# Kernel optimization log

Measured on AMD Instinct MI355X. Metric: run time of the kernel, lower is better.

## Reference

```python
import jax, jax.numpy as jnp
import numpy as np

N = 100000   # nodes
E = 1600000  # edges
G = 512      # graphs in batch
F_IN = 30
H = 128
EPS = 1e-5   # BatchNorm1d default eps


def setup_inputs() -> dict:
    key = jax.random.key(0)
    ks = jax.random.split(key, 16)
    x = jax.random.normal(ks[0], (N, F_IN), dtype=jnp.float32)
    edge_index = jax.random.randint(ks[1], (2, E), 0, N, dtype=jnp.int64)
    batch = jnp.sort(jax.random.randint(ks[2], (N,), 0, G, dtype=jnp.int64))
    d = {"x": x, "edge_index": edge_index, "batch": batch}
    dims = [(F_IN, H), (H, H), (H, H)]
    for i, (din, dout) in enumerate(dims):
        d[f"W{i}"] = jax.random.normal(ks[3 + i], (din, dout), dtype=jnp.float32) * (1.0 / np.sqrt(din))
        d[f"b{i}"] = jnp.zeros((dout,), dtype=jnp.float32)
        d[f"g{i}"] = jnp.ones((dout,), dtype=jnp.float32)   # BN gamma
        d[f"bt{i}"] = jnp.zeros((dout,), dtype=jnp.float32)  # BN beta
    d["HW1"] = jax.random.normal(ks[9], (H, 64), dtype=jnp.float32) * (1.0 / np.sqrt(H))
    d["Hb1"] = jnp.zeros((64,), dtype=jnp.float32)
    d["HW2"] = jax.random.normal(ks[10], (64, 1), dtype=jnp.float32) * 0.125
    d["Hb2"] = jnp.zeros((1,), dtype=jnp.float32)
    return d


def _bn(x, gamma, beta):
    # training-mode BatchNorm1d over node dim, biased variance (as torch uses for normalization)
    mu = jnp.mean(x, axis=0)
    var = jnp.mean(jnp.square(x - mu), axis=0)
    return (x - mu) * jax.lax.rsqrt(var + EPS) * gamma + beta


def reference(x, edge_index, batch, W0, b0, g0, bt0, W1, b1, g1, bt1, W2, b2, g2, bt2, HW1, Hb1, HW2, Hb2):
    # GCNConv: add self-loops, symmetric D^{-1/2}(A+I)D^{-1/2} normalization
    loop = jnp.arange(N, dtype=edge_index.dtype)
    src = jnp.concatenate([edge_index[0], loop])  # [E+N]
    dst = jnp.concatenate([edge_index[1], loop])
    deg = jax.ops.segment_sum(jnp.ones(src.shape, jnp.float32), dst, num_segments=N)
    dinv = jax.lax.rsqrt(jnp.maximum(deg, 1.0))  # deg >= 1 due to self-loops
    norm = (dinv[src] * dinv[dst])[:, None]      # [E+N, 1]

    for W, b, g, bt in ((W0, b0, g0, bt0), (W1, b1, g1, bt1), (W2, b2, g2, bt2)):
        h = x @ W                                           # [N, H]
        agg = jax.ops.segment_sum(h[src] * norm, dst, num_segments=N) + b
        x = jnp.maximum(_bn(agg, g, bt), 0.0)               # BN + ReLU (dropout = identity here)

    # global_mean_pool over graph ids
    counts = jax.ops.segment_sum(jnp.ones((N,), jnp.float32), batch, num_segments=G)
    pooled = jax.ops.segment_sum(x, batch, num_segments=G) / jnp.maximum(counts, 1.0)[:, None]

    h = jnp.maximum(pooled @ HW1 + Hb1, 0.0)
    return (h @ HW2 + Hb2).squeeze(-1)  # [G]
```

## Files before the change

### kernel.cpp

```cpp
#include <hip/hip_runtime.h>

#define BN_EPS 1e-5f
#define BSH 8

typedef __attribute__((ext_vector_type(8))) short bf16x8;
typedef __attribute__((ext_vector_type(4))) float f32x4;

__device__ inline float bfhi(unsigned int v) { return __uint_as_float(v & 0xFFFF0000u); }
__device__ inline float bflo(unsigned int v) { return __uint_as_float(v << 16); }
__device__ inline unsigned short f2bf(float f) {
  unsigned int u = __float_as_uint(f);
  u += 0x7FFFu + ((u >> 16) & 1u);
  return (unsigned short)(u >> 16);
}
__device__ inline unsigned int pack2bf(float lo, float hi) {
  return (unsigned int)f2bf(lo) | ((unsigned int)f2bf(hi) << 16);
}

__global__ void k_prep(const int* __restrict__ src, const int* __restrict__ dst,
                       int* __restrict__ gcur, uint2* __restrict__ sedge,
                       int NB, int CAP, int E, int BB,
                       const float* __restrict__ x, const float* __restrict__ W0,
                       const float* __restrict__ W1, const float* __restrict__ W2,
                       unsigned short* __restrict__ xb, unsigned short* __restrict__ Wt0,
                       unsigned short* __restrict__ Wt1, unsigned short* __restrict__ Wt2,
                       int n) {
  if ((int)blockIdx.x < BB) {
    __shared__ int lh[512], rb[512];
    int tid = threadIdx.x;
    for (int i = tid; i < NB; i += 256) lh[i] = 0;
    __syncthreads();
    int base = blockIdx.x * 8192;
    int lim = min(8192, E - base);
    for (int i = tid; i < lim; i += 256)
      atomicAdd(&lh[dst[base + i] >> BSH], 1);
    __syncthreads();
    for (int i = tid; i < NB; i += 256) {
      int c = lh[i];
      rb[i] = c ? atomicAdd(&gcur[i], c) : 0;
      lh[i] = 0;
    }
    __syncthreads();
    for (int i = tid; i < lim; i += 256) {
      int d = dst[base + i];
      int s = src[base + i];
      int b = d >> BSH;
      int pos = rb[b] + atomicAdd(&lh[b], 1);
      if (pos < CAP) {
        uint2 v; v.x = (unsigned int)s; v.y = (unsigned int)d;
        sedge[(size_t)b * CAP + pos] = v;
      }
    }
  } else {
    int t0 = (((int)blockIdx.x - BB) * 256 + (int)threadIdx.x) * 4;
#pragma unroll
    for (int u = 0; u < 4; ++u) {
      int t = t0 + u;
      if (t < 4096) {
        int nn = t >> 5, k = t & 31;
        Wt0[t] = f2bf(k < 30 ? W0[k * 128 + nn] : 0.f);
      } else if (t < 20480) {
        int i = t - 4096; int nn = i >> 7, k = i & 127;
        Wt1[i] = f2bf(W1[k * 128 + nn]);
      } else if (t < 36864) {
        int i = t - 20480; int nn = i >> 7, k = i & 127;
        Wt2[i] = f2bf(W2[k * 128 + nn]);
      } else {
        int i = t - 36864;
        if (i < n * 32) {
          int row = i >> 5, c = i & 31;
          xb[i] = f2bf(c < 30 ? x[row * 30 + c] : 0.f);
        }
      }
    }
  }
}

__global__ void k_csr1(const uint2* __restrict__ sedge, const int* __restrict__ gcur,
                       int* __restrict__ startv, int* __restrict__ cnt,
                       float* __restrict__ dinv, int CAP, int n) {
  int b = blockIdx.x, tid = threadIdx.x;
  __shared__ int h[256], sc[256];
  if (tid < 256) h[tid] = 0;
  __syncthreads();
  int cb = gcur[b]; if (cb > CAP) cb = CAP;
  const uint2* sd = sedge + (size_t)b * CAP;
  for (int i = tid; i < cb; i += 1024) atomicAdd(&h[sd[i].y & 255], 1);
  __syncthreads();
  if (tid < 256) sc[tid] = h[tid];
  __syncthreads();
  for (int o = 1; o < 256; o <<= 1) {
    int t = (tid < 256 && tid >= o) ? sc[tid - o] : 0;
    __syncthreads();
    if (tid < 256) sc[tid] += t;
    __syncthreads();
  }
  if (tid < 256) {
    int gd = (b << BSH) + tid;
    if (gd < n) {
      int v = h[tid];
      startv[gd] = b * CAP + (sc[tid] - v);
      cnt[gd] = v;
      dinv[gd] = rsqrtf((float)v + 1.0f);
    }
  }
}

__global__ void k_csr2(const uint2* __restrict__ sedge, const int* __restrict__ gcur,
                       const int* __restrict__ startv, const float* __restrict__ dinv,
                       unsigned int* __restrict__ elist, int CAP, int n) {
  int b = blockIdx.x, tid = threadIdx.x;
  __shared__ int cur[256];
  if (tid < 256) {
    int gd = (b << BSH) + tid;
    cur[tid] = (gd < n) ? startv[gd] : 0;
  }
  __syncthreads();
  int cb = gcur[b]; if (cb > CAP) cb = CAP;
  const uint2* sd = sedge + (size_t)b * CAP;
  for (int i = tid; i < cb; i += 1024) {
    uint2 e = sd[i];
    int pos = atomicAdd(&cur[e.y & 255], 1);
    unsigned int u = (unsigned int)(dinv[e.x] * 32767.0f + 0.5f);
    elist[pos] = e.x | (u << 17);
  }
}

__global__ void k_gather0(const unsigned int* __restrict__ elist, const int* __restrict__ start,
                          const int* __restrict__ cnt, const float* __restrict__ dinv,
                          const uint4* __restrict__ x4,
                          unsigned int* __restrict__ G0, int n) {
  int lane = threadIdx.x & 63;
  int wv   = threadIdx.x >> 6;
  int grp  = lane >> 2;
  int q4   = lane & 3;
  int row  = blockIdx.x * 4 + wv;
  bool active = row < n;

  float acc[8];
  float di = 0.f, dq = 0.f;
  int len = 0;
  const unsigned int* ep = elist;
  if (active) {
    di = dinv[row];
    dq = di * (1.0f / 32767.0f);
    len = cnt[row];
    ep = elist + start[row];
  }
  {
    float selfw = (grp == 0 && active) ? di * di : 0.f;
    uint4 hv = (grp == 0 && active) ? x4[(size_t)row * 4 + q4] : make_uint4(0, 0, 0, 0);
    acc[0] = bflo(hv.x) * selfw; acc[1] = bfhi(hv.x) * selfw;
    acc[2] = bflo(hv.y) * selfw; acc[3] = bfhi(hv.y) * selfw;
    acc[4] = bflo(hv.z) * selfw; acc[5] = bfhi(hv.z) * selfw;
    acc[6] = bflo(hv.w) * selfw; acc[7] = bfhi(hv.w) * selfw;
  }
  int j = 0;
  for (; j + 32 <= len; j += 32) {
    unsigned int e0 = ep[j + grp];
    unsigned int e1 = ep[j + 16 + grp];
    uint4 v0 = x4[(size_t)(e0 & 0x1FFFFu) * 4 + q4];
    uint4 v1 = x4[(size_t)(e1 & 0x1FFFFu) * 4 + q4];
    float w0 = (float)(e0 >> 17) * dq;
    float w1 = (float)(e1 >> 17) * dq;
    acc[0] = fmaf(bflo(v0.x), w0, acc[0]); acc[1] = fmaf(bfhi(v0.x), w0, acc[1]);
    acc[2] = fmaf(bflo(v0.y), w0, acc[2]); acc[3] = fmaf(bfhi(v0.y), w0, acc[3]);
    acc[4] = fmaf(bflo(v0.z), w0, acc[4]); acc[5] = fmaf(bfhi(v0.z), w0, acc[5]);
    acc[6] = fmaf(bflo(v0.w), w0, acc[6]); acc[7] = fmaf(bfhi(v0.w), w0, acc[7]);
    acc[0] = fmaf(bflo(v1.x), w1, acc[0]); acc[1] = fmaf(bfhi(v1.x), w1, acc[1]);
    acc[2] = fmaf(bflo(v1.y), w1, acc[2]); acc[3] = fmaf(bfhi(v1.y), w1, acc[3]);
    acc[4] = fmaf(bflo(v1.z), w1, acc[4]); acc[5] = fmaf(bfhi(v1.z), w1, acc[5]);
    acc[6] = fmaf(bflo(v1.w), w1, acc[6]); acc[7] = fmaf(bfhi(v1.w), w1, acc[7]);
  }
  for (; j < len; j += 16) {
    int jj = j + grp;
    unsigned int e = (jj < len) ? ep[jj] : 0u;
    uint4 v = x4[(size_t)(e & 0x1FFFFu) * 4 + q4];
    float w = (float)(e >> 17) * dq;
    acc[0] = fmaf(bflo(v.x), w, acc[0]); acc[1] = fmaf(bfhi(v.x), w, acc[1]);
    acc[2] = fmaf(bflo(v.y), w, acc[2]); acc[3] = fmaf(bfhi(v.y), w, acc[3]);
    acc[4] = fmaf(bflo(v.z), w, acc[4]); acc[5] = fmaf(bfhi(v.z), w, acc[5]);
    acc[6] = fmaf(bflo(v.w), w, acc[6]); acc[7] = fmaf(bfhi(v.w), w, acc[7]);
  }
#pragma unroll
  for (int k = 0; k < 8; ++k) {
    acc[k] += __shfl_xor(acc[k], 4);
    acc[k] += __shfl_xor(acc[k], 8);
    acc[k] += __shfl_xor(acc[k], 16);
    acc[k] += __shfl_xor(acc[k], 32);
  }
  if (grp == 0 && active) {
    uint4 o;
    o.x = pack2bf(acc[0], acc[1]);
    o.y = pack2bf(acc[2], acc[3]);
    o.z = pack2bf(acc[4], acc[5]);
    o.w = pack2bf(acc[6], acc[7]);
    ((uint4*)G0)[(size_t)row * 4 + q4] = o;
  }
}

template <int KP, bool DOBN, bool DOSTATS>
__global__ void k_gemm_mfma(const unsigned short* __restrict__ A,
                            const unsigned short* __restrict__ Wt,
                            const float* __restrict__ bnIn, const float* __restrict__ gamma,
                            const float* __restrict__ beta,
                            const float* __restrict__ bias, float* __restrict__ bnslab,
                            unsigned short* __restrict__ C, int n) {
  __shared__ float ssc[128], ssh[128];
  if constexpr (DOBN) {
    __shared__ float red[256];
    int tid = threadIdx.x;
    int which = tid >> 7, c = tid & 127;
    float s = 0.f;
    for (int k = 0; k < 64; ++k) s += bnIn[k * 256 + which * 128 + c];
    red[tid] = s;
    __syncthreads();
    if (tid < 128) {
      float invn = 1.0f / (float)n;
      float mu  = red[tid] * invn;
      float var = fmaxf(red[128 + tid] * invn - mu * mu, 0.f);
      float sc  = gamma[tid] * rsqrtf(var + BN_EPS);
      ssc[tid] = sc;
      ssh[tid] = fmaf(-mu, sc, beta[tid]);
    }
    __syncthreads();
  }
  int wave = threadIdx.x >> 6;
  int lane = threadIdx.x & 63;
  int m0 = blockIdx.x * 128 + wave * 32;
  int lm = lane & 15;
  int lq = lane >> 4;

  f32x4 acc[2][8] = {};
  const unsigned short* Arow0 = A + (size_t)(m0 + lm) * KP + lq * 8;
  const unsigned short* Arow1 = Arow0 + (size_t)16 * KP;
  const unsigned short* Bbase = Wt + (size_t)lm * KP + lq * 8;

#pragma unroll
  for (int k0 = 0; k0 < KP; k0 += 32) {
    uint4 ra0 = *(const uint4*)(Arow0 + k0);
    uint4 ra1 = *(const uint4*)(Arow1 + k0);
    bf16x8 a0, a1;
    if constexpr (DOBN) {
      int cb = k0 + lq * 8;
      unsigned int w0 = pack2bf(fmaxf(fmaf(bflo(ra0.x), ssc[cb+0], ssh[cb+0]), 0.f),
                                fmaxf(fmaf(bfhi(ra0.x), ssc[cb+1], ssh[cb+1]), 0.f));
      unsigned int w1 = pack2bf(fmaxf(fmaf(bflo(ra0.y), ssc[cb+2], ssh[cb+2]), 0.f),
                                fmaxf(fmaf(bfhi(ra0.y), ssc[cb+3], ssh[cb+3]), 0.f));
      unsigned int w2 = pack2bf(fmaxf(fmaf(bflo(ra0.z), ssc[cb+4], ssh[cb+4]), 0.f),
                                fmaxf(fmaf(bfhi(ra0.z), ssc[cb+5], ssh[cb+5]), 0.f));
      unsigned int w3 = pack2bf(fmaxf(fmaf(bflo(ra0.w), ssc[cb+6], ssh[cb+6]), 0.f),
                                fmaxf(fmaf(bfhi(ra0.w), ssc[cb+7], ssh[cb+7]), 0.f));
      uint4 pa0 = make_uint4(w0, w1, w2, w3);
      a0 = *(bf16x8*)&pa0;
      unsigned int y0 = pack2bf(fmaxf(fmaf(bflo(ra1.x), ssc[cb+0], ssh[cb+0]), 0.f),
                                fmaxf(fmaf(bfhi(ra1.x), ssc[cb+1], ssh[cb+1]), 0.f));
      unsigned int y1 = pack2bf(fmaxf(fmaf(bflo(ra1.y), ssc[cb+2], ssh[cb+2]), 0.f),
                                fmaxf(fmaf(bfhi(ra1.y), ssc[cb+3], ssh[cb+3]), 0.f));
      unsigned int y2 = pack2bf(fmaxf(fmaf(bflo(ra1.z), ssc[cb+4], ssh[cb+4]), 0.f),
                                fmaxf(fmaf(bfhi(ra1.z), ssc[cb+5], ssh[cb+5]), 0.f));
      unsigned int y3 = pack2bf(fmaxf(fmaf(bflo(ra1.w), ssc[cb+6], ssh[cb+6]), 0.f),
                                fmaxf(fmaf(bfhi(ra1.w), ssc[cb+7], ssh[cb+7]), 0.f));
      uint4 pa1 = make_uint4(y0, y1, y2, y3);
      a1 = *(bf16x8*)&pa1;
    } else {
      a0 = *(bf16x8*)&ra0;
      a1 = *(bf16x8*)&ra1;
    }
#pragma unroll
    for (int t = 0; t < 8; ++t) {
      bf16x8 b = *(const bf16x8*)(Bbase + (size_t)t * 16 * KP + k0);
      acc[0][t] = __builtin_amdgcn_mfma_f32_16x16x32_bf16(a0, b, acc[0][t], 0, 0, 0);
      acc[1][t] = __builtin_amdgcn_mfma_f32_16x16x32_bf16(a1, b, acc[1][t], 0, 0, 0);
    }
  }

#pragma unroll
  for (int h = 0; h < 2; ++h) {
    int rbase = m0 + h * 16 + lq * 4;
#pragma unroll
    for (int t = 0; t < 8; ++t) {
      int col = t * 16 + lm;
      float bv = DOSTATS ? bias[col] : 0.f;
#pragma unroll
      for (int r = 0; r < 4; ++r) {
        int row = rbase + r;
        if (row < n) C[(size_t)row * 128 + col] = f2bf(acc[h][t][r] + bv);
      }
    }
  }

  if constexpr (DOSTATS) {
    __shared__ float sms[4][256];
#pragma unroll
    for (int t = 0; t < 8; ++t) {
      int col = t * 16 + lm;
      float bv = bias[col];
      float s = 0.f, s2 = 0.f;
#pragma unroll
      for (int h = 0; h < 2; ++h) {
        int rbase = m0 + h * 16 + lq * 4;
#pragma unroll
        for (int r = 0; r < 4; ++r) {
          if (rbase + r < n) {
            float v = acc[h][t][r] + bv;
            s += v; s2 = fmaf(v, v, s2);
          }
        }
      }
      s  += __shfl_xor(s, 16);  s  += __shfl_xor(s, 32);
      s2 += __shfl_xor(s2, 16); s2 += __shfl_xor(s2, 32);
      if (lq == 0) { sms[wave][col] = s; sms[wave][128 + col] = s2; }
    }
    __syncthreads();
    int tid = threadIdx.x;
    int slab = (blockIdx.x & 63) * 256;
    float tot = sms[0][tid] + sms[1][tid] + sms[2][tid] + sms[3][tid];
    atomicAdd(&bnslab[slab + tid], tot);
  }
}

__global__ void k_gather(const unsigned int* __restrict__ elist, const int* __restrict__ start,
                         const int* __restrict__ cnt, const float* __restrict__ dinv,
                         const uint4* __restrict__ h4,
                         const float* __restrict__ bias, unsigned int* __restrict__ agg,
                         float* __restrict__ bnsumP, int n) {
  int lane = threadIdx.x & 63;
  int wv   = threadIdx.x >> 6;
  int grp  = lane >> 4;
  int c8   = lane & 15;
  int row  = blockIdx.x * 4 + wv;
  bool active = row < n;

  float acc[8];
  float di = 0.f, dq = 0.f;
  int len = 0;
  const unsigned int* ep = elist;

  if (active) {
    di = dinv[row];
    dq = di * (1.0f / 32767.0f);
    len = cnt[row];
    ep = elist + start[row];
  }

  {
    float selfw = (grp == 0 && active) ? di * di : 0.f;
    float4 b0 = make_float4(0.f, 0.f, 0.f, 0.f), b1 = b0;
    if (grp == 0 && active) {
      b0 = ((const float4*)bias)[c8 * 2];
      b1 = ((const float4*)bias)[c8 * 2 + 1];
    }
    uint4 hv = active ? h4[(size_t)row * 16 + c8] : make_uint4(0, 0, 0, 0);
    acc[0] = fmaf(bflo(hv.x), selfw, b0.x);
    acc[1] = fmaf(bfhi(hv.x), selfw, b0.y);
    acc[2] = fmaf(bflo(hv.y), selfw, b0.z);
    acc[3] = fmaf(bfhi(hv.y), selfw, b0.w);
    acc[4] = fmaf(bflo(hv.z), selfw, b1.x);
    acc[5] = fmaf(bfhi(hv.z), selfw, b1.y);
    acc[6] = fmaf(bflo(hv.w), selfw, b1.z);
    acc[7] = fmaf(bfhi(hv.w), selfw, b1.w);
  }

  int j = 0;
  for (; j + 16 <= len; j += 16) {
    unsigned int e0 = ep[j + grp];
    unsigned int e1 = ep[j + 4 + grp];
    unsigned int e2 = ep[j + 8 + grp];
    unsigned int e3 = ep[j + 12 + grp];
    uint4 v0 = h4[(size_t)(e0 & 0x1FFFFu) * 16 + c8];
    uint4 v1 = h4[(size_t)(e1 & 0x1FFFFu) * 16 + c8];
    uint4 v2 = h4[(size_t)(e2 & 0x1FFFFu) * 16 + c8];
    uint4 v3 = h4[(size_t)(e3 & 0x1FFFFu) * 16 + c8];
    float w0 = (float)(e0 >> 17) * dq;
    float w1 = (float)(e1 >> 17) * dq;
    float w2 = (float)(e2 >> 17) * dq;
    float w3 = (float)(e3 >> 17) * dq;
    acc[0] = fmaf(bflo(v0.x), w0, acc[0]); acc[1] = fmaf(bfhi(v0.x), w0, acc[1]);
    acc[2] = fmaf(bflo(v0.y), w0, acc[2]); acc[3] = fmaf(bfhi(v0.y), w0, acc[3]);
    acc[4] = fmaf(bflo(v0.z), w0, acc[4]); acc[5] = fmaf(bfhi(v0.z), w0, acc[5]);
    acc[6] = fmaf(bflo(v0.w), w0, acc[6]); acc[7] = fmaf(bfhi(v0.w), w0, acc[7]);
    acc[0] = fmaf(bflo(v1.x), w1, acc[0]); acc[1] = fmaf(bfhi(v1.x), w1, acc[1]);
    acc[2] = fmaf(bflo(v1.y), w1, acc[2]); acc[3] = fmaf(bfhi(v1.y), w1, acc[3]);
    acc[4] = fmaf(bflo(v1.z), w1, acc[4]); acc[5] = fmaf(bfhi(v1.z), w1, acc[5]);
    acc[6] = fmaf(bflo(v1.w), w1, acc[6]); acc[7] = fmaf(bfhi(v1.w), w1, acc[7]);
    acc[0] = fmaf(bflo(v2.x), w2, acc[0]); acc[1] = fmaf(bfhi(v2.x), w2, acc[1]);
    acc[2] = fmaf(bflo(v2.y), w2, acc[2]); acc[3] = fmaf(bfhi(v2.y), w2, acc[3]);
    acc[4] = fmaf(bflo(v2.z), w2, acc[4]); acc[5] = fmaf(bfhi(v2.z), w2, acc[5]);
    acc[6] = fmaf(bflo(v2.w), w2, acc[6]); acc[7] = fmaf(bfhi(v2.w), w2, acc[7]);
    acc[0] = fmaf(bflo(v3.x), w3, acc[0]); acc[1] = fmaf(bfhi(v3.x), w3, acc[1]);
    acc[2] = fmaf(bflo(v3.y), w3, acc[2]); acc[3] = fmaf(bfhi(v3.y), w3, acc[3]);
    acc[4] = fmaf(bflo(v3.z), w3, acc[4]); acc[5] = fmaf(bfhi(v3.z), w3, acc[5]);
    acc[6] = fmaf(bflo(v3.w), w3, acc[6]); acc[7] = fmaf(bfhi(v3.w), w3, acc[7]);
  }
  for (; j + 8 <= len; j += 8) {
    unsigned int e0 = ep[j + grp];
    unsigned int e1 = ep[j + 4 + grp];
    uint4 v0 = h4[(size_t)(e0 & 0x1FFFFu) * 16 + c8];
    uint4 v1 = h4[(size_t)(e1 & 0x1FFFFu) * 16 + c8];
    float w0 = (float)(e0 >> 17) * dq;
    float w1 = (float)(e1 >> 17) * dq;
    acc[0] = fmaf(bflo(v0.x), w0, acc[0]); acc[1] = fmaf(bfhi(v0.x), w0, acc[1]);
    acc[2] = fmaf(bflo(v0.y), w0, acc[2]); acc[3] = fmaf(bfhi(v0.y), w0, acc[3]);
    acc[4] = fmaf(bflo(v0.z), w0, acc[4]); acc[5] = fmaf(bfhi(v0.z), w0, acc[5]);
    acc[6] = fmaf(bflo(v0.w), w0, acc[6]); acc[7] = fmaf(bfhi(v0.w), w0, acc[7]);
    acc[0] = fmaf(bflo(v1.x), w1, acc[0]); acc[1] = fmaf(bfhi(v1.x), w1, acc[1]);
    acc[2] = fmaf(bflo(v1.y), w1, acc[2]); acc[3] = fmaf(bfhi(v1.y), w1, acc[3]);
    acc[4] = fmaf(bflo(v1.z), w1, acc[4]); acc[5] = fmaf(bfhi(v1.z), w1, acc[5]);
    acc[6] = fmaf(bflo(v1.w), w1, acc[6]); acc[7] = fmaf(bfhi(v1.w), w1, acc[7]);
  }
  for (; j < len; j += 4) {
    int jj = j + grp;
    unsigned int e = (jj < len) ? ep[jj] : 0u;
    uint4 v = h4[(size_t)(e & 0x1FFFFu) * 16 + c8];
    float w = (float)(e >> 17) * dq;
    acc[0] = fmaf(bflo(v.x), w, acc[0]); acc[1] = fmaf(bfhi(v.x), w, acc[1]);
    acc[2] = fmaf(bflo(v.y), w, acc[2]); acc[3] = fmaf(bfhi(v.y), w, acc[3]);
    acc[4] = fmaf(bflo(v.z), w, acc[4]); acc[5] = fmaf(bfhi(v.z), w, acc[5]);
    acc[6] = fmaf(bflo(v.w), w, acc[6]); acc[7] = fmaf(bfhi(v.w), w, acc[7]);
  }

#pragma unroll
  for (int k = 0; k < 8; ++k) {
    acc[k] += __shfl_xor(acc[k], 16);
    acc[k] += __shfl_xor(acc[k], 32);
  }

  __shared__ float sm[2][4][128];
  if (lane < 16) {
    if (active) {
      uint4 o;
      o.x = pack2bf(acc[0], acc[1]);
      o.y = pack2bf(acc[2], acc[3]);
      o.z = pack2bf(acc[4], acc[5]);
      o.w = pack2bf(acc[6], acc[7]);
      ((uint4*)agg)[(size_t)row * 16 + c8] = o;
    }
#pragma unroll
    for (int k = 0; k < 8; ++k) {
      float a = acc[k];
      sm[0][wv][c8 * 8 + k] = a;
      sm[1][wv][c8 * 8 + k] = a * a;
    }
  }
  __syncthreads();
  int tid = threadIdx.x;
  int slab = (blockIdx.x & 63) * 256;
  if (tid < 128) {
    float s = sm[0][0][tid] + sm[0][1][tid] + sm[0][2][tid] + sm[0][3][tid];
    atomicAdd(&bnsumP[slab + tid], s);
  } else {
    int c = tid - 128;
    float s = sm[1][0][c] + sm[1][1][c] + sm[1][2][c] + sm[1][3][c];
    atomicAdd(&bnsumP[slab + 128 + c], s);
  }
}

__global__ void k_poolhead(const unsigned int* __restrict__ aggd, const float* __restrict__ bnIn,
                           const float* __restrict__ gamma, const float* __restrict__ beta,
                           const int* __restrict__ batch, const float* __restrict__ HW1,
                           const float* __restrict__ Hb1, const float* __restrict__ HW2,
                           const float* __restrict__ Hb2, float* __restrict__ out, int n) {
  __shared__ float bsc[128], bsh[128];
  {
    __shared__ float red[256];
    int tid = threadIdx.x;
    int which = tid >> 7, c = tid & 127;
    float s = 0.f;
    for (int k = 0; k < 64; ++k) s += bnIn[k * 256 + which * 128 + c];
    red[tid] = s;
    __syncthreads();
    if (tid < 128) {
      float invn = 1.0f / (float)n;
      float mu  = red[tid] * invn;
      float var = fmaxf(red[128 + tid] * invn - mu * mu, 0.f);
      float sc  = gamma[tid] * rsqrtf(var + BN_EPS);
      bsc[tid] = sc;
      bsh[tid] = fmaf(-mu, sc, beta[tid]);
    }
    __syncthreads();
  }
  int g = blockIdx.x;
  int wv = threadIdx.x >> 6, t = threadIdx.x & 63;
  int lo = 0, hi = n;
  while (lo < hi) { int mid = (lo + hi) >> 1; if (batch[mid] < g) lo = mid + 1; else hi = mid; }
  int s = lo;
  lo = 0; hi = n;
  int g1 = g + 1;
  while (lo < hi) { int mid = (lo + hi) >> 1; if (batch[mid] < g1) lo = mid + 1; else hi = mid; }
  int e = lo;

  int c16 = t & 31;
  int rpar = t >> 5;
  float sc0 = bsc[4 * c16], sc1 = bsc[4 * c16 + 1];
  float sc2 = bsc[4 * c16 + 2], sc3 = bsc[4 * c16 + 3];
  float sh0 = bsh[4 * c16], sh1 = bsh[4 * c16 + 1];
  float sh2 = bsh[4 * c16 + 2], sh3 = bsh[4 * c16 + 3];
  float a0 = 0.f, a1 = 0.f, a2 = 0.f, a3 = 0.f;
  for (int i = s + wv * 2 + rpar; i < e; i += 8) {
    uint2 u = ((const uint2*)aggd)[(size_t)i * 32 + c16];
    a0 += fmaxf(fmaf(bflo(u.x), sc0, sh0), 0.f);
    a1 += fmaxf(fmaf(bfhi(u.x), sc1, sh1), 0.f);
    a2 += fmaxf(fmaf(bflo(u.y), sc2, sh2), 0.f);
    a3 += fmaxf(fmaf(bfhi(u.y), sc3, sh3), 0.f);
  }
  a0 += __shfl_xor(a0, 32);
  a1 += __shfl_xor(a1, 32);
  a2 += __shfl_xor(a2, 32);
  a3 += __shfl_xor(a3, 32);
  __shared__ float pp[4][128];
  if (t < 32) {
    pp[wv][4 * c16]     = a0;
    pp[wv][4 * c16 + 1] = a1;
    pp[wv][4 * c16 + 2] = a2;
    pp[wv][4 * c16 + 3] = a3;
  }
  __syncthreads();
  if (wv == 0) {
    float inv = 1.0f / fmaxf((float)(e - s), 1.f);
    float p0 = (pp[0][2 * t] + pp[1][2 * t] + pp[2][2 * t] + pp[3][2 * t]) * inv;
    float p1 = (pp[0][2 * t + 1] + pp[1][2 * t + 1] + pp[2][2 * t + 1] + pp[3][2 * t + 1]) * inv;
    pp[0][2 * t] = p0;
    pp[0][2 * t + 1] = p1;
    float acc = Hb1[t];
    for (int k = 0; k < 128; ++k) acc = fmaf(pp[0][k], HW1[k * 64 + t], acc);
    float v = fmaxf(acc, 0.f) * HW2[t];
    for (int off = 32; off > 0; off >>= 1) v += __shfl_down(v, off);
    if (t == 0) out[g] = v + Hb2[0];
  }
}

extern "C" void kernel_launch(void* const* d_in, const int* in_sizes, int n_in,
                              void* d_out, int out_size, void* d_ws, size_t ws_size,
                              hipStream_t stream) {
  const int F_IN = 30, H = 128;
  const float* x   = (const float*)d_in[0];
  const int* eidx  = (const int*)d_in[1];
  const int* batch = (const int*)d_in[2];
  const int N = in_sizes[0] / F_IN;
  const int E = in_sizes[1] / 2;
  const int G = out_size;
  const int* srcp = eidx;
  const int* dstp = eidx + E;
  const float* HW1 = (const float*)d_in[15];
  const float* Hb1 = (const float*)d_in[16];
  const float* HW2 = (const float*)d_in[17];
  const float* Hb2 = (const float*)d_in[18];
  float* outp = (float*)d_out;

  const int Npad = (N + 127) & ~127;
  size_t nh = (size_t)Npad * H;
  const int NB = (N + 255) >> BSH;
  const int CAP = ((E / NB) * 3) / 2 + 128;
  const int NBpad = (NB + 63) & ~63;

  unsigned short* bufH = (unsigned short*)d_ws;
  unsigned short* bufX = bufH + nh;
  unsigned short* xbf  = bufX + nh;
  unsigned short* G0   = xbf + (size_t)Npad * 32;
  float* dinv = (float*)(G0 + (size_t)Npad * 32);
  int*   cnt    = (int*)(dinv + N);
  int*   startv = cnt + N;
  int*   gcur   = startv + N;
  float* bnsumP = (float*)(gcur + NBpad);
  unsigned short* Wt0 = (unsigned short*)(bnsumP + 3 * 64 * 256);
  unsigned short* Wt1 = Wt0 + 128 * 32;
  unsigned short* Wt2 = Wt1 + 128 * 128;
  unsigned int* elist = (unsigned int*)(Wt2 + 128 * 128 + 64);
  uint2* sedge = (uint2*)bufX;

  hipMemsetAsync(gcur, 0, ((size_t)NBpad + 3 * 64 * 256) * sizeof(int), stream);

  const int BB = (E + 8191) / 8192;
  const int TT = 36864 + N * 32;
  const int CV = (TT + 1023) >> 10;
  k_prep<<<BB + CV, 256, 0, stream>>>(srcp, dstp, gcur, sedge, NB, CAP, E, BB,
                                      x, (const float*)d_in[3], (const float*)d_in[7],
                                      (const float*)d_in[11], xbf, Wt0, Wt1, Wt2, N);
  k_csr1<<<NB, 1024, 0, stream>>>(sedge, gcur, startv, cnt, dinv, CAP, N);
  k_csr2<<<NB, 1024, 0, stream>>>(sedge, gcur, startv, dinv, elist, CAP, N);

  const float* b0  = (const float*)d_in[4];
  const float* gm0 = (const float*)d_in[5];
  const float* bt0 = (const float*)d_in[6];
  const float* b1  = (const float*)d_in[8];
  const float* gm1 = (const float*)d_in[9];
  const float* bt1 = (const float*)d_in[10];
  const float* b2  = (const float*)d_in[12];
  const float* gm2 = (const float*)d_in[13];
  const float* bt2 = (const float*)d_in[14];

  float* slab0 = bnsumP;
  float* slab1 = bnsumP + (size_t)1 * 64 * 256;
  float* slab2 = bnsumP + (size_t)2 * 64 * 256;

  k_gather0<<<(N + 3) / 4, 256, 0, stream>>>(elist, startv, cnt, dinv,
                                             (const uint4*)xbf, (unsigned int*)G0, N);
  k_gemm_mfma<32, false, true><<<Npad / 128, 256, 0, stream>>>(
      G0, Wt0, nullptr, nullptr, nullptr, b0, slab0, bufX, N);

  k_gemm_mfma<128, true, false><<<Npad / 128, 256, 0, stream>>>(
      bufX, Wt1, slab0, gm0, bt0, nullptr, nullptr, bufH, N);
  k_gather<<<(N + 3) / 4, 256, 0, stream>>>(elist, startv, cnt, dinv,
                                            (const uint4*)bufH, b1,
                                            (unsigned int*)bufX, slab1, N);

  k_gemm_mfma<128, true, false><<<Npad / 128, 256, 0, stream>>>(
      bufX, Wt2, slab1, gm1, bt1, nullptr, nullptr, bufH, N);
  k_gather<<<(N + 3) / 4, 256, 0, stream>>>(elist, startv, cnt, dinv,
                                            (const uint4*)bufH, b2,
                                            (unsigned int*)bufX, slab2, N);

  k_poolhead<<<G, 256, 0, stream>>>((const unsigned int*)bufX, slab2, gm2, bt2, batch,
                                    HW1, Hb1, HW2, Hb2, outp, N);
}
```

Baseline: 419.9 us.

## Compute degrees with global atomics in prep and merge CSR kernels

Per-node in-degree counts are now produced with global atomics during the bucketing pass in k_prep, so the separate CSR counting kernel that re-read the bucketed edges is gone. The two CSR kernels are fused into one that scans the counts, writes start offsets and dinv, then scatters edges, recomputing the source's dinv from its count instead of reading dinv written by another block. This removes one launch and a full pass over the staged edge list. In exchange it adds 1.6M global atomics on random addresses and a larger memset.

```diff
diff --git a/kernel.cpp b/kernel.cpp
--- a/kernel.cpp
+++ b/kernel.cpp
@@ -18,7 +18,8 @@
 }
 
 __global__ void k_prep(const int* __restrict__ src, const int* __restrict__ dst,
-                       int* __restrict__ gcur, uint2* __restrict__ sedge,
+                       int* __restrict__ gcur, int* __restrict__ cnt,
+                       uint2* __restrict__ sedge,
                        int NB, int CAP, int E, int BB,
                        const float* __restrict__ x, const float* __restrict__ W0,
                        const float* __restrict__ W1, const float* __restrict__ W2,
@@ -32,8 +33,11 @@
     __syncthreads();
     int base = blockIdx.x * 8192;
     int lim = min(8192, E - base);
-    for (int i = tid; i < lim; i += 256)
-      atomicAdd(&lh[dst[base + i] >> BSH], 1);
+    for (int i = tid; i < lim; i += 256) {
+      int d = dst[base + i];
+      atomicAdd(&lh[d >> BSH], 1);
+      atomicAdd(&cnt[d], 1);
+    }
     __syncthreads();
     for (int i = tid; i < NB; i += 256) {
       int c = lh[i];
@@ -76,18 +80,18 @@
   }
 }
 
-__global__ void k_csr1(const uint2* __restrict__ sedge, const int* __restrict__ gcur,
-                       int* __restrict__ startv, int* __restrict__ cnt,
-                       float* __restrict__ dinv, int CAP, int n) {
+__global__ void k_csr(const uint2* __restrict__ sedge, const int* __restrict__ gcur,
+                      const int* __restrict__ cnt, int* __restrict__ startv,
+                      float* __restrict__ dinv, unsigned int* __restrict__ elist,
+                      int CAP, int n) {
   int b = blockIdx.x, tid = threadIdx.x;
-  __shared__ int h[256], sc[256];
-  if (tid < 256) h[tid] = 0;
-  __syncthreads();
-  int cb = gcur[b]; if (cb > CAP) cb = CAP;
-  const uint2* sd = sedge + (size_t)b * CAP;
-  for (int i = tid; i < cb; i += 1024) atomicAdd(&h[sd[i].y & 255], 1);
-  __syncthreads();
-  if (tid < 256) sc[tid] = h[tid];
+  __shared__ int sc[256], cur[256];
+  int v = 0;
+  if (tid < 256) {
+    int gd = (b << BSH) + tid;
+    v = (gd < n) ? cnt[gd] : 0;
+    sc[tid] = v;
+  }
   __syncthreads();
   for (int o = 1; o < 256; o <<= 1) {
     int t = (tid < 256 && tid >= o) ? sc[tid - o] : 0;
@@ -97,23 +101,12 @@
   }
   if (tid < 256) {
     int gd = (b << BSH) + tid;
+    int st = b * CAP + (sc[tid] - v);
+    cur[tid] = st;
     if (gd < n) {
-      int v = h[tid];
-      startv[gd] = b * CAP + (sc[tid] - v);
-      cnt[gd] = v;
+      startv[gd] = st;
       dinv[gd] = rsqrtf((float)v + 1.0f);
     }
-  }
-}
-
-__global__ void k_csr2(const uint2* __restrict__ sedge, const int* __restrict__ gcur,
-                       const int* __restrict__ startv, const float* __restrict__ dinv,
-                       unsigned int* __restrict__ elist, int CAP, int n) {
-  int b = blockIdx.x, tid = threadIdx.x;
-  __shared__ int cur[256];
-  if (tid < 256) {
-    int gd = (b << BSH) + tid;
-    cur[tid] = (gd < n) ? startv[gd] : 0;
   }
   __syncthreads();
   int cb = gcur[b]; if (cb > CAP) cb = CAP;
@@ -121,7 +114,8 @@
   for (int i = tid; i < cb; i += 1024) {
     uint2 e = sd[i];
     int pos = atomicAdd(&cur[e.y & 255], 1);
-    unsigned int u = (unsigned int)(dinv[e.x] * 32767.0f + 0.5f);
+    float ds = rsqrtf((float)cnt[e.x] + 1.0f);
+    unsigned int u = (unsigned int)(ds * 32767.0f + 0.5f);
     elist[pos] = e.x | (u << 17);
   }
 }
@@ -559,26 +553,25 @@
   unsigned short* xbf  = bufX + nh;
   unsigned short* G0   = xbf + (size_t)Npad * 32;
   float* dinv = (float*)(G0 + (size_t)Npad * 32);
-  int*   cnt    = (int*)(dinv + N);
-  int*   startv = cnt + N;
+  int*   startv = (int*)(dinv + N);
   int*   gcur   = startv + N;
-  float* bnsumP = (float*)(gcur + NBpad);
+  int*   cnt    = gcur + NBpad;
+  float* bnsumP = (float*)(cnt + N);
   unsigned short* Wt0 = (unsigned short*)(bnsumP + 3 * 64 * 256);
   unsigned short* Wt1 = Wt0 + 128 * 32;
   unsigned short* Wt2 = Wt1 + 128 * 128;
   unsigned int* elist = (unsigned int*)(Wt2 + 128 * 128 + 64);
   uint2* sedge = (uint2*)bufX;
 
-  hipMemsetAsync(gcur, 0, ((size_t)NBpad + 3 * 64 * 256) * sizeof(int), stream);
+  hipMemsetAsync(gcur, 0, ((size_t)NBpad + N + 3 * 64 * 256) * sizeof(int), stream);
 
   const int BB = (E + 8191) / 8192;
   const int TT = 36864 + N * 32;
   const int CV = (TT + 1023) >> 10;
-  k_prep<<<BB + CV, 256, 0, stream>>>(srcp, dstp, gcur, sedge, NB, CAP, E, BB,
+  k_prep<<<BB + CV, 256, 0, stream>>>(srcp, dstp, gcur, cnt, sedge, NB, CAP, E, BB,
                                       x, (const float*)d_in[3], (const float*)d_in[7],
                                       (const float*)d_in[11], xbf, Wt0, Wt1, Wt2, N);
-  k_csr1<<<NB, 1024, 0, stream>>>(sedge, gcur, startv, cnt, dinv, CAP, N);
-  k_csr2<<<NB, 1024, 0, stream>>>(sedge, gcur, startv, dinv, elist, CAP, N);
+  k_csr<<<NB, 1024, 0, stream>>>(sedge, gcur, cnt, startv, dinv, elist, CAP, N);
 
   const float* b0  = (const float*)d_in[4];
   const float* gm0 = (const float*)d_in[5];
```

Result: slower. 471.2 us (+12.2%).
